# Performance work log

Measured on AMD Instinct MI355X. Metric: run time of the kernel, lower is better.

The kernel has to match this reference:

```python
import jax, jax.numpy as jnp
import numpy as np

L, D, H, T, DFF = 4, 1024, 8, 1000, 4096
HS = D // H  # 128


def _rope_cos_sin():
    # theta_i = 10000^(-2(i-1)/dim) for i in 1..dim/2 (dim = head size)
    i = jnp.arange(1, HS // 2 + 1, dtype=jnp.float32)
    theta = jnp.power(jnp.float32(10000.0), -2.0 * (i - 1.0) / HS)
    t = jnp.arange(T, dtype=jnp.float32)
    ang = t[:, None] * theta[None, :]              # (T, HS/2)
    return jnp.cos(ang), jnp.sin(ang)


def _apply_rope(x, cos, sin):
    # x: (B,H,T,HS); interpret last dim as HS/2 complex pairs and multiply by e^{i t theta}
    xs = x.reshape(*x.shape[:-1], HS // 2, 2)
    xr, xi = xs[..., 0], xs[..., 1]
    c = cos[None, None, :, :]
    s = sin[None, None, :, :]
    out_r = xr * c - xi * s
    out_i = xr * s + xi * c
    return jnp.stack([out_r, out_i], axis=-1).reshape(x.shape)


def _ln(x, g, b, eps=1e-5):
    m = jnp.mean(x, axis=-1, keepdims=True)
    v = jnp.mean((x - m) ** 2, axis=-1, keepdims=True)
    return (x - m) * jax.lax.rsqrt(v + eps) * g + b


def setup_inputs() -> dict:
    key = jax.random.key(0)
    ks = jax.random.split(key, 16)
    sc = 0.02
    inp = {
        'x':   jax.random.normal(ks[0], (8, T, D), jnp.float32),
        'Wq':  sc * jax.random.normal(ks[1], (L, D, D), jnp.float32),
        'Wk':  sc * jax.random.normal(ks[2], (L, D, D), jnp.float32),
        'Wv':  sc * jax.random.normal(ks[3], (L, D, D), jnp.float32),
        'Wpk': sc * jax.random.normal(ks[4], (L, T, T), jnp.float32),
        'bpk': jnp.zeros((L, T), jnp.float32),
        'Wpv': sc * jax.random.normal(ks[5], (L, T, T), jnp.float32),
        'bpv': jnp.zeros((L, T), jnp.float32),
        'ln1_g': jnp.ones((L, D), jnp.float32),
        'ln1_b': jnp.zeros((L, D), jnp.float32),
        'W1':  sc * jax.random.normal(ks[6], (L, DFF, D), jnp.float32),
        'b1':  jnp.zeros((L, DFF), jnp.float32),
        'W2':  sc * jax.random.normal(ks[7], (L, D, DFF), jnp.float32),
        'b2':  jnp.zeros((L, D), jnp.float32),
        'ln2_g': jnp.ones((L, D), jnp.float32),
        'ln2_b': jnp.zeros((L, D), jnp.float32),
    }
    return inp


def reference(x, Wq, Wk, Wv, Wpk, bpk, Wpv, bpv, ln1_g, ln1_b,
              W1, b1, W2, b2, ln2_g, ln2_b):
    B = x.shape[0]
    cos, sin = _rope_cos_sin()
    out = x
    for l in range(L):
        src = out
        # QKV projections (bias=False), split into heads: (B,H,T,HS)
        q = jnp.einsum('btc,dc->btd', src, Wq[l]).reshape(B, T, H, HS).transpose(0, 2, 1, 3)
        k = jnp.einsum('btc,dc->btd', src, Wk[l]).reshape(B, T, H, HS).transpose(0, 2, 1, 3)
        v = jnp.einsum('btc,dc->btd', src, Wv[l]).reshape(B, T, H, HS).transpose(0, 2, 1, 3)
        # ChunkedLinear over the SEQUENCE axis for K and V (single 1000x1000 block)
        k = jnp.einsum('bhtd,ut->bhud', k, Wpk[l]) + bpk[l][None, None, :, None]
        v = jnp.einsum('bhtd,ut->bhud', v, Wpv[l]) + bpv[l][None, None, :, None]
        # RoPE on q and k
        q = _apply_rope(q, cos, sin)
        k = _apply_rope(k, cos, sin)
        # Full (non-causal; mask is commented out in source) softmax attention
        scores = jnp.einsum('bhqd,bhkd->bhqk', q, k) / jnp.sqrt(jnp.float32(HS))
        attn = jax.nn.softmax(scores, axis=-1)
        y = jnp.einsum('bhqk,bhkd->bhqd', attn, v)
        y = y.transpose(0, 2, 1, 3).reshape(B, T, D)  # NOTE: no output proj (faithful to source)
        src = _ln(src + y, ln1_g[l], ln1_b[l])
        h = jax.nn.gelu(jnp.einsum('btd,fd->btf', src, W1[l]) + b1[l], approximate=False)
        src = _ln(src + jnp.einsum('btf,df->btd', h, W2[l]) + b2[l], ln2_g[l], ln2_b[l])
        out = src
    return out
```

## Files before the change

### kernel.cpp

```cpp
#include <hip/hip_runtime.h>
#include <cstdint>
#include <cstddef>


typedef unsigned short u16;
typedef unsigned int u32;
typedef __attribute__((ext_vector_type(8))) short s16x8;
typedef __attribute__((ext_vector_type(4))) float f32x4;
typedef __attribute__((ext_vector_type(4))) unsigned short u16x4;

#define DEV static __device__ __forceinline__

DEV float bf2f(u16 u) { union { u32 u; float f; } v; v.u = ((u32)u) << 16; return v.f; }
DEV u16 f2bf(float f) {
  union { float f; u32 u; } v; v.f = f;
  return (u16)((v.u + 0x7fffu + ((v.u >> 16) & 1u)) >> 16);
}

#define MFMA(acc_, a_, b_) \
  asm volatile("v_mfma_f32_16x16x32_bf16 %0, %1, %2, %0" : "+v"(acc_) : "v"(a_), "v"(b_))

#define GLD16(g_, l_) \
  __builtin_amdgcn_global_load_lds((const __attribute__((address_space(1))) void*)(g_), \
                                   (__attribute__((address_space(3))) void*)(l_), 16, 0, 0)

static constexpr int T_ = 1000, D_ = 1024, H_ = 8, HS_ = 128, B_ = 8;
static constexpr int BT_ = B_ * T_;

DEV void rope8(s16x8& v, const float* __restrict__ ct, const float* __restrict__ st,
               int t, int i0) {
  const f32x4 c4 = *(const f32x4*)(ct + t * 64 + i0);
  const f32x4 s4 = *(const f32x4*)(st + t * 64 + i0);
#pragma unroll
  for (int p = 0; p < 4; ++p) {
    const float xr = bf2f((u16)v[2 * p]), xi = bf2f((u16)v[2 * p + 1]);
    v[2 * p]     = (short)f2bf(xr * c4[p] - xi * s4[p]);
    v[2 * p + 1] = (short)f2bf(xr * s4[p] + xi * c4[p]);
  }
}

__global__ void tab_kernel(float* __restrict__ ct, float* __restrict__ st) {
  const int id = blockIdx.x * 256 + threadIdx.x;
  const int i = id & 63, t = id >> 6;
  const float theta = powf(10000.f, -(float)i * (1.f / 64.f));
  const float ang = (float)t * theta;
  ct[id] = cosf(ang);
  st[id] = sinf(ang);
}

__global__ void convert_kernel(const float* __restrict__ in, u16* __restrict__ out, int n) {
  const int i = (blockIdx.x * 256 + threadIdx.x) * 4;
  if (i < n) {
    const float4 v = *(const float4*)(in + i);
    uint2 pk;
    pk.x = (u32)f2bf(v.x) | ((u32)f2bf(v.y) << 16);
    pk.y = (u32)f2bf(v.z) | ((u32)f2bf(v.w) << 16);
    *(uint2*)(out + i) = pk;
  }
}

__global__ void zerotail_kernel(u16* __restrict__ KTg, u16* __restrict__ VTg,
                                u16* __restrict__ Vmt) {
  const int id = blockIdx.x * 256 + threadIdx.x;
  if (id >= 3 * 8192 * 24) return;
  const int which = id / 196608, rem = id % 196608;
  const int bd = rem / 24, t = 1000 + rem % 24;
  u16* p = (which == 0) ? KTg : (which == 1) ? VTg : Vmt;
  p[(size_t)bd * 1024 + t] = 0;
}

template <int BIAS, bool ACT, bool OUTBF, bool SPLIT>
__global__ __launch_bounds__(256) void gemm2p(
    const u16* __restrict__ A, const u16* __restrict__ B, void* __restrict__ Cv,
    const float* __restrict__ bias, u16* __restrict__ KT, u16* __restrict__ VT,
    int M, int N, int K, int lda, int ldb, int ldc, long sA, long sB, long sC) {
  __shared__ alignas(16) u16 As[2][4096];
  __shared__ alignas(16) u16 Bs[2][4096];
  const int z = blockIdx.z;
  A += (size_t)z * (size_t)sA;
  B += (size_t)z * (size_t)sB;
  const int m0 = blockIdx.y * 128, n0 = blockIdx.x * 128;
  const int tid = threadIdx.x;
  const int wid = tid >> 6, lane = tid & 63;
  const int wr = wid >> 1, wc = wid & 1;
  const int l15 = lane & 15, l4 = lane >> 4;
  const int srow = tid >> 2;
  const int sg = ((tid & 3) ^ ((tid >> 3) & 3)) << 3;
  const u16* gA0 = A + (size_t)min(m0 + srow, M - 1) * lda + sg;
  const u16* gA1 = A + (size_t)min(m0 + 64 + srow, M - 1) * lda + sg;
  const u16* gB0 = B + (size_t)min(n0 + srow, N - 1) * ldb + sg;
  const u16* gB1 = B + (size_t)min(n0 + 64 + srow, N - 1) * ldb + sg;
  const int gg = (l4 ^ ((l15 >> 1) & 3)) << 3;
  const int aBase = (wr * 64 + l15) * 32 + gg;
  const int bBase = (wc * 64 + l15) * 32 + gg;

  f32x4 acc[4][4] = {};
  const int KT_n = K >> 5;
  GLD16(gA0, &As[0][tid * 8]);
  GLD16(gA1, &As[0][(256 + tid) * 8]);
  GLD16(gB0, &Bs[0][tid * 8]);
  GLD16(gB1, &Bs[0][(256 + tid) * 8]);
  __syncthreads();
  int cur = 0;
#pragma unroll 1
  for (int kt = 0; kt < KT_n; ++kt) {
    if (kt + 1 < KT_n) {
      const int kb = (kt + 1) << 5;
      GLD16(gA0 + kb, &As[cur ^ 1][tid * 8]);
      GLD16(gA1 + kb, &As[cur ^ 1][(256 + tid) * 8]);
      GLD16(gB0 + kb, &Bs[cur ^ 1][tid * 8]);
      GLD16(gB1 + kb, &Bs[cur ^ 1][(256 + tid) * 8]);
    }
    s16x8 af[4], bfr[4];
#pragma unroll
    for (int i = 0; i < 4; ++i) af[i] = *(const s16x8*)&As[cur][aBase + i * 512];
#pragma unroll
    for (int i = 0; i < 4; ++i) bfr[i] = *(const s16x8*)&Bs[cur][bBase + i * 512];
    __builtin_amdgcn_s_setprio(1);
#pragma unroll
    for (int mi = 0; mi < 4; ++mi)
#pragma unroll
      for (int ni = 0; ni < 4; ++ni) MFMA(acc[mi][ni], af[mi], bfr[ni]);
    __builtin_amdgcn_s_setprio(0);
    __syncthreads();
    cur ^= 1;
  }
  asm volatile("s_nop 7\n\ts_nop 7"
               : "+v"(acc[3][0]), "+v"(acc[3][1]), "+v"(acc[3][2]), "+v"(acc[3][3]));
  if constexpr (SPLIT) {
#pragma unroll
    for (int mi = 0; mi < 4; ++mi) {
      const int rb = m0 + wr * 64 + mi * 16 + l4 * 4;
      if (rb < M) {
#pragma unroll
        for (int ni = 0; ni < 4; ++ni) {
          const int colg = n0 + wc * 64 + ni * 16 + l15;
          if (colg < 1024) {
#pragma unroll
            for (int r = 0; r < 4; ++r)
              ((u16*)Cv)[(size_t)(rb + r) * 1024 + colg] = f2bf(acc[mi][ni][r]);
          } else {
            u16* dst = (colg < 2048) ? KT : VT;
            const int dcol = colg & 1023;
            const int bq = rb / 1000;
            const int tq = rb - bq * 1000;
            u16x4 pk;
#pragma unroll
            for (int r = 0; r < 4; ++r) pk[r] = f2bf(acc[mi][ni][r]);
            *(u16x4*)(dst + (size_t)bq * 1048576 + (size_t)dcol * 1024 + tq) = pk;
          }
        }
      }
    }
  } else {
#pragma unroll
    for (int mi = 0; mi < 4; ++mi) {
#pragma unroll
      for (int ni = 0; ni < 4; ++ni) {
        const int colg = n0 + wc * 64 + ni * 16 + l15;
#pragma unroll
        for (int r = 0; r < 4; ++r) {
          const int rowg = m0 + wr * 64 + mi * 16 + l4 * 4 + r;
          if (rowg < M && colg < N) {
            float v = acc[mi][ni][r];
            if (BIAS == 1) v += bias[rowg];
            if (BIAS == 2) v += bias[colg];
            if (ACT) v = 0.5f * v * (1.0f + erff(v * 0.70710678118654752f));
            const size_t idx = (size_t)z * (size_t)sC + (size_t)rowg * ldc + colg;
            if (OUTBF) ((u16*)Cv)[idx] = f2bf(v);
            else       ((float*)Cv)[idx] = v;
          }
        }
      }
    }
  }
}

__global__ __launch_bounds__(256) void attn_kernel(const u16* __restrict__ Q,
                                                   const u16* __restrict__ Km,
                                                   const u16* __restrict__ Vmt,
                                                   u16* __restrict__ Y,
                                                   const float* __restrict__ ct,
                                                   const float* __restrict__ st) {
  __shared__ alignas(16) u16 Ks[64][136];
  __shared__ alignas(16) u16 Vts[128][72];
  __shared__ alignas(16) u16 Ps[4][32][72];
  const int qt = blockIdx.x;
  const int bh = blockIdx.y;
  const int b = bh >> 3, h = bh & 7;
  const int tid = threadIdx.x;
  const int w = tid >> 6, lane = tid & 63;
  const int l15 = lane & 15, l4 = lane >> 4;
  const size_t qbase = (size_t)b * 1000 * 1024 + h * HS_;
  const size_t kbase = (size_t)b * 1024000 + h * HS_;
  const size_t vbase = (size_t)b * 1048576 + (size_t)(h * HS_) * 1024;
  const int q0 = qt * 128 + w * 32;
  s16x8 aq[2][4];
#pragma unroll
  for (int qf = 0; qf < 2; ++qf) {
    const int qrow = q0 + qf * 16 + l15;
#pragma unroll
    for (int c = 0; c < 4; ++c) {
      s16x8 v = {};
      if (qrow < T_) {
        v = *(const s16x8*)(Q + qbase + (size_t)qrow * 1024 + c * 32 + l4 * 8);
        rope8(v, ct, st, qrow, c * 16 + l4 * 4);
      }
      aq[qf][c] = v;
    }
  }
  f32x4 acc[2][8] = {};
  float m_run[2][4], l_run[2][4];
#pragma unroll
  for (int qf = 0; qf < 2; ++qf)
#pragma unroll
    for (int r = 0; r < 4; ++r) { m_run[qf][r] = -1e30f; l_run[qf][r] = 0.f; }
  const float SCALE = 0.08838834764831845f;
  for (int kt = 0; kt < 16; ++kt) {
    {
      const int r = tid >> 2, c0 = (tid & 3) << 5;
      const int kk = kt * 64 + r;
#pragma unroll
      for (int v = 0; v < 4; ++v) {
        s16x8 val = {};
        if (kk < T_) {
          val = *(const s16x8*)(Km + kbase + (size_t)kk * 1024 + c0 + v * 8);
          rope8(val, ct, st, kk, (c0 + v * 8) >> 1);
        }
        *(s16x8*)&Ks[r][c0 + v * 8] = val;
      }
      const int r2 = tid >> 1, c2s = (tid & 1) << 5;
#pragma unroll
      for (int v = 0; v < 4; ++v) {
        const s16x8 val = *(const s16x8*)(Vmt + vbase + (size_t)r2 * 1024 + kt * 64 + c2s + v * 8);
        *(s16x8*)&Vts[r2][c2s + v * 8] = val;
      }
    }
    __syncthreads();
    f32x4 sacc[2][4] = {};
#pragma unroll
    for (int c = 0; c < 4; ++c) {
      s16x8 bk[4];
#pragma unroll
      for (int f = 0; f < 4; ++f) bk[f] = *(const s16x8*)&Ks[f * 16 + l15][c * 32 + l4 * 8];
#pragma unroll
      for (int qf = 0; qf < 2; ++qf)
#pragma unroll
        for (int f = 0; f < 4; ++f) MFMA(sacc[qf][f], aq[qf][c], bk[f]);
    }
    asm volatile("s_nop 7\n\ts_nop 7"
                 : "+v"(sacc[0][0]), "+v"(sacc[0][1]), "+v"(sacc[0][2]), "+v"(sacc[0][3]),
                   "+v"(sacc[1][0]), "+v"(sacc[1][1]), "+v"(sacc[1][2]), "+v"(sacc[1][3]));
#pragma unroll
    for (int qf = 0; qf < 2; ++qf) {
      float sv[4][4];
#pragma unroll
      for (int f = 0; f < 4; ++f) {
        const int key = kt * 64 + f * 16 + l15;
#pragma unroll
        for (int r = 0; r < 4; ++r) sv[f][r] = (key < T_) ? sacc[qf][f][r] * SCALE : -1e30f;
      }
#pragma unroll
      for (int r = 0; r < 4; ++r) {
        float mx = fmaxf(fmaxf(sv[0][r], sv[1][r]), fmaxf(sv[2][r], sv[3][r]));
#pragma unroll
        for (int off = 8; off >= 1; off >>= 1) mx = fmaxf(mx, __shfl_xor(mx, off));
        const float mn = fmaxf(m_run[qf][r], mx);
        const float corr = __expf(m_run[qf][r] - mn);
        m_run[qf][r] = mn;
        float rs = 0.f;
#pragma unroll
        for (int f = 0; f < 4; ++f) {
          const float p = __expf(sv[f][r] - mn);
          rs += p;
          Ps[w][qf * 16 + l4 * 4 + r][f * 16 + l15] = f2bf(p);
        }
#pragma unroll
        for (int off = 8; off >= 1; off >>= 1) rs += __shfl_xor(rs, off);
        l_run[qf][r] = l_run[qf][r] * corr + rs;
#pragma unroll
        for (int n = 0; n < 8; ++n) acc[qf][n][r] *= corr;
      }
    }
    asm volatile("s_waitcnt lgkmcnt(0)" ::: "memory");
#pragma unroll
    for (int c2 = 0; c2 < 2; ++c2) {
      s16x8 pa[2];
#pragma unroll
      for (int qf = 0; qf < 2; ++qf)
        pa[qf] = *(const s16x8*)&Ps[w][qf * 16 + l15][c2 * 32 + l4 * 8];
#pragma unroll
      for (int n = 0; n < 8; ++n) {
        const s16x8 vb = *(const s16x8*)&Vts[n * 16 + l15][c2 * 32 + l4 * 8];
#pragma unroll
        for (int qf = 0; qf < 2; ++qf) MFMA(acc[qf][n], pa[qf], vb);
      }
    }
    __syncthreads();
  }
  asm volatile("s_nop 7\n\ts_nop 7"
               : "+v"(acc[0][6]), "+v"(acc[0][7]), "+v"(acc[1][6]), "+v"(acc[1][7]));
#pragma unroll
  for (int qf = 0; qf < 2; ++qf)
#pragma unroll
    for (int n = 0; n < 8; ++n)
#pragma unroll
      for (int r = 0; r < 4; ++r) {
        const int q = q0 + qf * 16 + l4 * 4 + r;
        if (q < T_)
          Y[(size_t)(b * 1000 + q) * 1024 + h * HS_ + n * 16 + l15] =
              f2bf(acc[qf][n][r] / l_run[qf][r]);
      }
}

__global__ __launch_bounds__(256) void addln_kernel(float* __restrict__ src,
                                                    const u16* __restrict__ add,
                                                    const float* __restrict__ g,
                                                    const float* __restrict__ bb,
                                                    u16* __restrict__ outb) {
  const int row = blockIdx.x;
  const int tid = threadIdx.x;
  const int d = tid * 4;
  float* s = src + (size_t)row * D_;
  const u16* a = add + (size_t)row * D_;
  f32x4 sv = *(const f32x4*)(s + d);
  const u16x4 av = *(const u16x4*)(a + d);
  float x[4];
  float sum = 0.f, sq = 0.f;
#pragma unroll
  for (int i = 0; i < 4; ++i) {
    const float v = sv[i] + bf2f(av[i]);
    x[i] = v; sum += v; sq += v * v;
  }
#pragma unroll
  for (int off = 32; off >= 1; off >>= 1) { sum += __shfl_xor(sum, off); sq += __shfl_xor(sq, off); }
  __shared__ float red[8];
  const int wid = tid >> 6;
  if ((tid & 63) == 0) { red[wid] = sum; red[4 + wid] = sq; }
  __syncthreads();
  sum = red[0] + red[1] + red[2] + red[3];
  sq = red[4] + red[5] + red[6] + red[7];
  const float mean = sum * (1.f / 1024.f);
  const float var = sq * (1.f / 1024.f) - mean * mean;
  const float rstd = rsqrtf(var + 1e-5f);
  const f32x4 gv = *(const f32x4*)(g + d);
  const f32x4 bv = *(const f32x4*)(bb + d);
  f32x4 yv;
  u16x4 ob;
#pragma unroll
  for (int i = 0; i < 4; ++i) {
    const float y = (x[i] - mean) * rstd * gv[i] + bv[i];
    yv[i] = y;
    ob[i] = f2bf(y);
  }
  *(f32x4*)(s + d) = yv;
  *(u16x4*)(outb + (size_t)row * D_ + d) = ob;
}

static inline int cdiv(int a, int b) { return (a + b - 1) / b; }

extern "C" void kernel_launch(void* const* d_in, const int* in_sizes, int n_in,
                              void* d_out, int out_size, void* d_ws, size_t ws_size,
                              hipStream_t stream) {
  const float* x    = (const float*)d_in[0];
  const float* Wq   = (const float*)d_in[1];
  const float* Wk   = (const float*)d_in[2];
  const float* Wv   = (const float*)d_in[3];
  const float* Wpk  = (const float*)d_in[4];
  const float* bpk  = (const float*)d_in[5];
  const float* Wpv  = (const float*)d_in[6];
  const float* bpv  = (const float*)d_in[7];
  const float* g1   = (const float*)d_in[8];
  const float* b1ln = (const float*)d_in[9];
  const float* W1   = (const float*)d_in[10];
  const float* b1   = (const float*)d_in[11];
  const float* W2   = (const float*)d_in[12];
  const float* b2   = (const float*)d_in[13];
  const float* g2   = (const float*)d_in[14];
  const float* b2ln = (const float*)d_in[15];

  char* wsb = (char*)d_ws;
  float* cosT = (float*)(wsb + 0);
  float* sinT = (float*)(wsb + 262144);
  float* srcf = (float*)(wsb + 524288);
  u16* srcb   = (u16*)(wsb + 33292288);
  u16* Qb     = (u16*)(wsb + 49676288);
  u16* KTg    = (u16*)(wsb + 66060288);
  u16* VTg    = (u16*)(wsb + 82837504);
  u16* Km     = (u16*)(wsb + 99614720);
  u16* Vmt    = (u16*)(wsb + 115998720);
  u16* yB     = (u16*)(wsb + 132775936);
  u16* wbuf   = (u16*)(wsb + 149159936);
  u16* hB     = Qb;

  u16* wqB  = wbuf + 0;
  u16* wpkB = wbuf + 3145728;
  u16* wpvB = wbuf + 4145728;
  u16* w1B  = wbuf + 5145728;
  u16* w2B  = wbuf + 9340032;

  tab_kernel<<<250, 256, 0, stream>>>(cosT, sinT);
  zerotail_kernel<<<2304, 256, 0, stream>>>(KTg, VTg, Vmt);
  hipMemcpyAsync(srcf, x, (size_t)BT_ * D_ * sizeof(float), hipMemcpyDeviceToDevice, stream);
  convert_kernel<<<cdiv(BT_ * D_, 1024), 256, 0, stream>>>(x, srcb, BT_ * D_);

  for (int l = 0; l < 4; ++l) {
    convert_kernel<<<cdiv(1048576, 1024), 256, 0, stream>>>(Wq + (size_t)l * 1048576, wqB, 1048576);
    convert_kernel<<<cdiv(1048576, 1024), 256, 0, stream>>>(Wk + (size_t)l * 1048576, wqB + 1048576, 1048576);
    convert_kernel<<<cdiv(1048576, 1024), 256, 0, stream>>>(Wv + (size_t)l * 1048576, wqB + 2097152, 1048576);
    convert_kernel<<<cdiv(1000000, 1024), 256, 0, stream>>>(Wpk + (size_t)l * 1000000, wpkB, 1000000);
    convert_kernel<<<cdiv(1000000, 1024), 256, 0, stream>>>(Wpv + (size_t)l * 1000000, wpvB, 1000000);
    convert_kernel<<<cdiv(4194304, 1024), 256, 0, stream>>>(W1 + (size_t)l * 4194304, w1B, 4194304);
    convert_kernel<<<cdiv(4194304, 1024), 256, 0, stream>>>(W2 + (size_t)l * 4194304, w2B, 4194304);

    gemm2p<0, false, true, true><<<dim3(24, 63, 1), 256, 0, stream>>>(
        srcb, wqB, Qb, nullptr, KTg, VTg, BT_, 3072, 1024, 1024, 1024, 1024, 0, 0, 0);

    gemm2p<1, false, true, false><<<dim3(8, 8, 8), 256, 0, stream>>>(
        wpkB, KTg, Km, bpk + (size_t)l * 1000, nullptr, nullptr,
        1000, 1024, 1024, 1000, 1024, 1024, 0L, 1048576L, 1024000L);

    gemm2p<2, false, true, false><<<dim3(8, 8, 8), 256, 0, stream>>>(
        VTg, wpvB, Vmt, bpv + (size_t)l * 1000, nullptr, nullptr,
        1024, 1000, 1024, 1024, 1000, 1024, 1048576L, 0L, 1048576L);

    attn_kernel<<<dim3(8, 64), 256, 0, stream>>>(Qb, Km, Vmt, yB, cosT, sinT);

    addln_kernel<<<BT_, 256, 0, stream>>>(srcf, yB, g1 + (size_t)l * 1024,
                                          b1ln + (size_t)l * 1024, srcb);

    gemm2p<2, true, true, false><<<dim3(32, 63, 1), 256, 0, stream>>>(
        srcb, w1B, hB, b1 + (size_t)l * 4096, nullptr, nullptr,
        BT_, 4096, 1024, 1024, 1024, 4096, 0, 0, 0);
    gemm2p<2, false, true, false><<<dim3(8, 63, 1), 256, 0, stream>>>(
        hB, w2B, yB, b2 + (size_t)l * 1024, nullptr, nullptr,
        BT_, 1024, 4096, 4096, 4096, 1024, 0, 0, 0);

    addln_kernel<<<BT_, 256, 0, stream>>>(srcf, yB, g2 + (size_t)l * 1024,
                                          b2ln + (size_t)l * 1024, srcb);
  }

  hipMemcpyAsync(d_out, srcf, (size_t)BT_ * D_ * sizeof(float), hipMemcpyDeviceToDevice, stream);
}
```

Measured before the change: 2.205 ms.

## Add 256x256 GEMM kernel with XCD-aware block remap and fuse K RoPE into projection

```diff
diff --git a/kernel.cpp b/kernel.cpp
--- a/kernel.cpp
+++ b/kernel.cpp
@@ -69,11 +69,124 @@
   p[(size_t)bd * 1024 + t] = 0;
 }
 
-template <int BIAS, bool ACT, bool OUTBF, bool SPLIT>
+template <int BMT, int BIAS, bool ACT, bool SPLIT>
+__global__ __launch_bounds__(512) void gemm256(
+    const u16* __restrict__ A, const u16* __restrict__ B, u16* __restrict__ Cv,
+    const float* __restrict__ bias, u16* __restrict__ KT, u16* __restrict__ VT,
+    int M, int N, int K, int lda, int ldb, int ldc, int cx, int cy, int ncx) {
+  constexpr int MI = 4 * BMT;
+  __shared__ alignas(16) u16 As[2][BMT * 4096];
+  __shared__ alignas(16) u16 Bs[2][8192];
+  int bx = blockIdx.x, by = blockIdx.y;
+  if (cx) {
+    const int lin = by * gridDim.x + bx;
+    const int xcd = lin & 7, c2 = lin >> 3;
+    bx = (xcd % ncx) * cx + c2 % cx;
+    by = (xcd / ncx) * cy + c2 / cx;
+  }
+  const int m0 = by * (BMT * 128), n0 = bx * 256;
+  const int tid = threadIdx.x;
+  const int wid = tid >> 6, lane = tid & 63;
+  const int wr = wid >> 2, wc = wid & 3;
+  const int l15 = lane & 15, l4 = lane >> 4;
+  const int srow = tid >> 2;
+  const int sg = ((tid & 3) ^ ((tid >> 3) & 3)) << 3;
+  const u16* gA[BMT];
+#pragma unroll
+  for (int j = 0; j < BMT; ++j)
+    gA[j] = A + (size_t)min(m0 + j * 128 + srow, M - 1) * lda + sg;
+  const u16* gB0 = B + (size_t)min(n0 + srow, N - 1) * ldb + sg;
+  const u16* gB1 = B + (size_t)min(n0 + 128 + srow, N - 1) * ldb + sg;
+  const int gg = (l4 ^ ((l15 >> 1) & 3)) << 3;
+  const int aBase = (wr * (BMT * 64) + l15) * 32 + gg;
+  const int bBase = (wc * 64 + l15) * 32 + gg;
+
+  f32x4 acc[MI][4] = {};
+  const int KTn = K >> 5;
+#pragma unroll
+  for (int j = 0; j < BMT; ++j) GLD16(gA[j], &As[0][j * 4096 + tid * 8]);
+  GLD16(gB0, &Bs[0][tid * 8]);
+  GLD16(gB1, &Bs[0][4096 + tid * 8]);
+  __syncthreads();
+  int cur = 0;
+#pragma unroll 1
+  for (int kt = 0; kt < KTn; ++kt) {
+    if (kt + 1 < KTn) {
+      const int kb = (kt + 1) << 5;
+#pragma unroll
+      for (int j = 0; j < BMT; ++j) GLD16(gA[j] + kb, &As[cur ^ 1][j * 4096 + tid * 8]);
+      GLD16(gB0 + kb, &Bs[cur ^ 1][tid * 8]);
+      GLD16(gB1 + kb, &Bs[cur ^ 1][4096 + tid * 8]);
+    }
+    s16x8 af[MI], bfr[4];
+#pragma unroll
+    for (int i = 0; i < MI; ++i) af[i] = *(const s16x8*)&As[cur][aBase + i * 512];
+#pragma unroll
+    for (int i = 0; i < 4; ++i) bfr[i] = *(const s16x8*)&Bs[cur][bBase + i * 512];
+    __builtin_amdgcn_s_setprio(1);
+#pragma unroll
+    for (int mi = 0; mi < MI; ++mi)
+#pragma unroll
+      for (int ni = 0; ni < 4; ++ni) MFMA(acc[mi][ni], af[mi], bfr[ni]);
+    __builtin_amdgcn_s_setprio(0);
+    __syncthreads();
+    cur ^= 1;
+  }
+  asm volatile("s_nop 7\n\ts_nop 7"
+               : "+v"(acc[MI - 1][0]), "+v"(acc[MI - 1][1]),
+                 "+v"(acc[MI - 1][2]), "+v"(acc[MI - 1][3]));
+  if constexpr (SPLIT) {
+#pragma unroll
+    for (int mi = 0; mi < MI; ++mi) {
+      const int rb = m0 + wr * (BMT * 64) + mi * 16 + l4 * 4;
+      if (rb < M) {
+#pragma unroll
+        for (int ni = 0; ni < 4; ++ni) {
+          const int colg = n0 + wc * 64 + ni * 16 + l15;
+          if (colg < 1024) {
+#pragma unroll
+            for (int r = 0; r < 4; ++r)
+              Cv[(size_t)(rb + r) * 1024 + colg] = f2bf(acc[mi][ni][r]);
+          } else {
+            u16* dst = (colg < 2048) ? KT : VT;
+            const int dcol = colg & 1023;
+            const int bq = rb / 1000;
+            const int tq = rb - bq * 1000;
+            u16x4 pk;
+#pragma unroll
+            for (int r = 0; r < 4; ++r) pk[r] = f2bf(acc[mi][ni][r]);
+            *(u16x4*)(dst + (size_t)bq * 1048576 + (size_t)dcol * 1024 + tq) = pk;
+          }
+        }
+      }
+    }
+  } else {
+#pragma unroll
+    for (int mi = 0; mi < MI; ++mi) {
+#pragma unroll
+      for (int ni = 0; ni < 4; ++ni) {
+        const int colg = n0 + wc * 64 + ni * 16 + l15;
+#pragma unroll
+        for (int r = 0; r < 4; ++r) {
+          const int rowg = m0 + wr * (BMT * 64) + mi * 16 + l4 * 4 + r;
+          if (rowg < M) {
+            float v = acc[mi][ni][r];
+            if (BIAS == 2) v += bias[colg];
+            if (ACT) v = 0.5f * v * (1.0f + erff(v * 0.70710678118654752f));
+            Cv[(size_t)rowg * ldc + colg] = f2bf(v);
+          }
+        }
+      }
+    }
+  }
+}
+
+template <int BIAS, bool ACT, bool OUTBF, bool RK>
 __global__ __launch_bounds__(256) void gemm2p(
     const u16* __restrict__ A, const u16* __restrict__ B, void* __restrict__ Cv,
-    const float* __restrict__ bias, u16* __restrict__ KT, u16* __restrict__ VT,
-    int M, int N, int K, int lda, int ldb, int ldc, long sA, long sB, long sC) {
+    const float* __restrict__ bias, const float* __restrict__ ct,
+    const float* __restrict__ st, int M, int N, int K, int lda, int ldb, int ldc,
+    long sA, long sB, long sC) {
   __shared__ alignas(16) u16 As[2][4096];
   __shared__ alignas(16) u16 Bs[2][4096];
   const int z = blockIdx.z;
@@ -95,7 +208,7 @@
   const int bBase = (wc * 64 + l15) * 32 + gg;
 
   f32x4 acc[4][4] = {};
-  const int KT_n = K >> 5;
+  const int KTn = K >> 5;
   GLD16(gA0, &As[0][tid * 8]);
   GLD16(gA1, &As[0][(256 + tid) * 8]);
   GLD16(gB0, &Bs[0][tid * 8]);
@@ -103,8 +216,8 @@
   __syncthreads();
   int cur = 0;
 #pragma unroll 1
-  for (int kt = 0; kt < KT_n; ++kt) {
-    if (kt + 1 < KT_n) {
+  for (int kt = 0; kt < KTn; ++kt) {
+    if (kt + 1 < KTn) {
       const int kb = (kt + 1) << 5;
       GLD16(gA0 + kb, &As[cur ^ 1][tid * 8]);
       GLD16(gA1 + kb, &As[cur ^ 1][(256 + tid) * 8]);
@@ -127,49 +240,29 @@
   }
   asm volatile("s_nop 7\n\ts_nop 7"
                : "+v"(acc[3][0]), "+v"(acc[3][1]), "+v"(acc[3][2]), "+v"(acc[3][3]));
-  if constexpr (SPLIT) {
-#pragma unroll
-    for (int mi = 0; mi < 4; ++mi) {
-      const int rb = m0 + wr * 64 + mi * 16 + l4 * 4;
-      if (rb < M) {
-#pragma unroll
-        for (int ni = 0; ni < 4; ++ni) {
-          const int colg = n0 + wc * 64 + ni * 16 + l15;
-          if (colg < 1024) {
-#pragma unroll
-            for (int r = 0; r < 4; ++r)
-              ((u16*)Cv)[(size_t)(rb + r) * 1024 + colg] = f2bf(acc[mi][ni][r]);
-          } else {
-            u16* dst = (colg < 2048) ? KT : VT;
-            const int dcol = colg & 1023;
-            const int bq = rb / 1000;
-            const int tq = rb - bq * 1000;
-            u16x4 pk;
-#pragma unroll
-            for (int r = 0; r < 4; ++r) pk[r] = f2bf(acc[mi][ni][r]);
-            *(u16x4*)(dst + (size_t)bq * 1048576 + (size_t)dcol * 1024 + tq) = pk;
-          }
+#pragma unroll
+  for (int mi = 0; mi < 4; ++mi) {
+#pragma unroll
+    for (int ni = 0; ni < 4; ++ni) {
+      const int colg = n0 + wc * 64 + ni * 16 + l15;
+#pragma unroll
+      for (int r = 0; r < 4; ++r) {
+        const int rowg = m0 + wr * 64 + mi * 16 + l4 * 4 + r;
+        float v = acc[mi][ni][r];
+        if (BIAS == 1) v += bias[min(rowg, M - 1)];
+        if (BIAS == 2) v += bias[colg];
+        if constexpr (RK) {
+          const int tt = min(rowg, T_ - 1);
+          const int ii = (colg & 127) >> 1;
+          const float c = ct[tt * 64 + ii], s = st[tt * 64 + ii];
+          const float partner = __shfl_xor(v, 1);
+          v = (colg & 1) ? (partner * s + v * c) : (v * c - partner * s);
         }
-      }
-    }
-  } else {
-#pragma unroll
-    for (int mi = 0; mi < 4; ++mi) {
-#pragma unroll
-      for (int ni = 0; ni < 4; ++ni) {
-        const int colg = n0 + wc * 64 + ni * 16 + l15;
-#pragma unroll
-        for (int r = 0; r < 4; ++r) {
-          const int rowg = m0 + wr * 64 + mi * 16 + l4 * 4 + r;
-          if (rowg < M && colg < N) {
-            float v = acc[mi][ni][r];
-            if (BIAS == 1) v += bias[rowg];
-            if (BIAS == 2) v += bias[colg];
-            if (ACT) v = 0.5f * v * (1.0f + erff(v * 0.70710678118654752f));
-            const size_t idx = (size_t)z * (size_t)sC + (size_t)rowg * ldc + colg;
-            if (OUTBF) ((u16*)Cv)[idx] = f2bf(v);
-            else       ((float*)Cv)[idx] = v;
-          }
+        if (ACT) v = 0.5f * v * (1.0f + erff(v * 0.70710678118654752f));
+        if (rowg < M && colg < N) {
+          const size_t idx = (size_t)z * (size_t)sC + (size_t)rowg * ldc + colg;
+          if (OUTBF) ((u16*)Cv)[idx] = f2bf(v);
+          else       ((float*)Cv)[idx] = v;
         }
       }
     }
@@ -223,10 +316,7 @@
 #pragma unroll
       for (int v = 0; v < 4; ++v) {
         s16x8 val = {};
-        if (kk < T_) {
-          val = *(const s16x8*)(Km + kbase + (size_t)kk * 1024 + c0 + v * 8);
-          rope8(val, ct, st, kk, (c0 + v * 8) >> 1);
-        }
+        if (kk < T_) val = *(const s16x8*)(Km + kbase + (size_t)kk * 1024 + c0 + v * 8);
         *(s16x8*)&Ks[r][c0 + v * 8] = val;
       }
       const int r2 = tid >> 1, c2s = (tid & 1) << 5;
@@ -413,11 +503,11 @@
     convert_kernel<<<cdiv(4194304, 1024), 256, 0, stream>>>(W1 + (size_t)l * 4194304, w1B, 4194304);
     convert_kernel<<<cdiv(4194304, 1024), 256, 0, stream>>>(W2 + (size_t)l * 4194304, w2B, 4194304);
 
-    gemm2p<0, false, true, true><<<dim3(24, 63, 1), 256, 0, stream>>>(
-        srcb, wqB, Qb, nullptr, KTg, VTg, BT_, 3072, 1024, 1024, 1024, 1024, 0, 0, 0);
-
-    gemm2p<1, false, true, false><<<dim3(8, 8, 8), 256, 0, stream>>>(
-        wpkB, KTg, Km, bpk + (size_t)l * 1000, nullptr, nullptr,
+    gemm256<2, 0, false, true><<<dim3(12, 32), 512, 0, stream>>>(
+        srcb, wqB, Qb, nullptr, KTg, VTg, BT_, 3072, 1024, 1024, 1024, 1024, 6, 8, 2);
+
+    gemm2p<1, false, true, true><<<dim3(8, 8, 8), 256, 0, stream>>>(
+        wpkB, KTg, Km, bpk + (size_t)l * 1000, cosT, sinT,
         1000, 1024, 1024, 1000, 1024, 1024, 0L, 1048576L, 1024000L);
 
     gemm2p<2, false, true, false><<<dim3(8, 8, 8), 256, 0, stream>>>(
@@ -429,10 +519,10 @@
     addln_kernel<<<BT_, 256, 0, stream>>>(srcf, yB, g1 + (size_t)l * 1024,
                                           b1ln + (size_t)l * 1024, srcb);
 
-    gemm2p<2, true, true, false><<<dim3(32, 63, 1), 256, 0, stream>>>(
+    gemm256<2, 2, true, false><<<dim3(16, 32), 512, 0, stream>>>(
         srcb, w1B, hB, b1 + (size_t)l * 4096, nullptr, nullptr,
-        BT_, 4096, 1024, 1024, 1024, 4096, 0, 0, 0);
-    gemm2p<2, false, true, false><<<dim3(8, 63, 1), 256, 0, stream>>>(
+        BT_, 4096, 1024, 1024, 1024, 4096, 8, 8, 2);
+    gemm256<1, 2, false, false><<<dim3(4, 63), 512, 0, stream>>>(
         hB, w2B, yB, b2 + (size_t)l * 1024, nullptr, nullptr,
         BT_, 1024, 4096, 4096, 4096, 1024, 0, 0, 0);
 
```

After: 2.611 ms. 18.4% more time.

## Fuse weight conversions, apply K RoPE in GEMM epilogue, MFMA row sums

Applied to the files above, without the earlier changes.

```diff
diff --git a/kernel.cpp b/kernel.cpp
--- a/kernel.cpp
+++ b/kernel.cpp
@@ -59,6 +59,29 @@
   }
 }
 
+__global__ __launch_bounds__(256) void convertL_kernel(
+    const float* __restrict__ Wq, const float* __restrict__ Wk, const float* __restrict__ Wv,
+    const float* __restrict__ Wpk, const float* __restrict__ Wpv,
+    const float* __restrict__ W1, const float* __restrict__ W2,
+    u16* __restrict__ wq, u16* __restrict__ wpk, u16* __restrict__ wpv,
+    u16* __restrict__ w1, u16* __restrict__ w2) {
+  const int i = blockIdx.x * 256 + threadIdx.x;
+  const float* src; u16* dst; int j;
+  if      (i <  262144) { src = Wq;  dst = wq;            j = i; }
+  else if (i <  524288) { src = Wk;  dst = wq + 1048576;  j = i -  262144; }
+  else if (i <  786432) { src = Wv;  dst = wq + 2097152;  j = i -  524288; }
+  else if (i < 1036432) { src = Wpk; dst = wpk;           j = i -  786432; }
+  else if (i < 1286432) { src = Wpv; dst = wpv;           j = i - 1036432; }
+  else if (i < 2335008) { src = W1;  dst = w1;            j = i - 1286432; }
+  else if (i < 3383584) { src = W2;  dst = w2;            j = i - 2335008; }
+  else return;
+  const float4 v = ((const float4*)src)[j];
+  uint2 pk;
+  pk.x = (u32)f2bf(v.x) | ((u32)f2bf(v.y) << 16);
+  pk.y = (u32)f2bf(v.z) | ((u32)f2bf(v.w) << 16);
+  ((uint2*)dst)[j] = pk;
+}
+
 __global__ void zerotail_kernel(u16* __restrict__ KTg, u16* __restrict__ VTg,
                                 u16* __restrict__ Vmt) {
   const int id = blockIdx.x * 256 + threadIdx.x;
@@ -69,10 +92,11 @@
   p[(size_t)bd * 1024 + t] = 0;
 }
 
-template <int BIAS, bool ACT, bool OUTBF, bool SPLIT>
+template <int BIAS, bool ACT, bool RK, bool SPLIT>
 __global__ __launch_bounds__(256) void gemm2p(
-    const u16* __restrict__ A, const u16* __restrict__ B, void* __restrict__ Cv,
-    const float* __restrict__ bias, u16* __restrict__ KT, u16* __restrict__ VT,
+    const u16* __restrict__ A, const u16* __restrict__ B, u16* __restrict__ Cv,
+    const float* __restrict__ bias, const float* __restrict__ ct,
+    const float* __restrict__ st, u16* __restrict__ KT, u16* __restrict__ VT,
     int M, int N, int K, int lda, int ldb, int ldc, long sA, long sB, long sC) {
   __shared__ alignas(16) u16 As[2][4096];
   __shared__ alignas(16) u16 Bs[2][4096];
@@ -95,7 +119,7 @@
   const int bBase = (wc * 64 + l15) * 32 + gg;
 
   f32x4 acc[4][4] = {};
-  const int KT_n = K >> 5;
+  const int KTn = K >> 5;
   GLD16(gA0, &As[0][tid * 8]);
   GLD16(gA1, &As[0][(256 + tid) * 8]);
   GLD16(gB0, &Bs[0][tid * 8]);
@@ -103,8 +127,8 @@
   __syncthreads();
   int cur = 0;
 #pragma unroll 1
-  for (int kt = 0; kt < KT_n; ++kt) {
-    if (kt + 1 < KT_n) {
+  for (int kt = 0; kt < KTn; ++kt) {
+    if (kt + 1 < KTn) {
       const int kb = (kt + 1) << 5;
       GLD16(gA0 + kb, &As[cur ^ 1][tid * 8]);
       GLD16(gA1 + kb, &As[cur ^ 1][(256 + tid) * 8]);
@@ -138,7 +162,7 @@
           if (colg < 1024) {
 #pragma unroll
             for (int r = 0; r < 4; ++r)
-              ((u16*)Cv)[(size_t)(rb + r) * 1024 + colg] = f2bf(acc[mi][ni][r]);
+              Cv[(size_t)(rb + r) * 1024 + colg] = f2bf(acc[mi][ni][r]);
           } else {
             u16* dst = (colg < 2048) ? KT : VT;
             const int dcol = colg & 1023;
@@ -161,15 +185,19 @@
 #pragma unroll
         for (int r = 0; r < 4; ++r) {
           const int rowg = m0 + wr * 64 + mi * 16 + l4 * 4 + r;
-          if (rowg < M && colg < N) {
-            float v = acc[mi][ni][r];
-            if (BIAS == 1) v += bias[rowg];
-            if (BIAS == 2) v += bias[colg];
-            if (ACT) v = 0.5f * v * (1.0f + erff(v * 0.70710678118654752f));
-            const size_t idx = (size_t)z * (size_t)sC + (size_t)rowg * ldc + colg;
-            if (OUTBF) ((u16*)Cv)[idx] = f2bf(v);
-            else       ((float*)Cv)[idx] = v;
+          float v = acc[mi][ni][r];
+          if (BIAS == 1) v += bias[min(rowg, M - 1)];
+          if (BIAS == 2) v += bias[min(colg, N - 1)];
+          if constexpr (RK) {
+            const int tt = min(rowg, T_ - 1);
+            const int ii = (colg & 127) >> 1;
+            const float c = ct[tt * 64 + ii], s = st[tt * 64 + ii];
+            const float partner = __shfl_xor(v, 1);
+            v = (colg & 1) ? (partner * s + v * c) : (v * c - partner * s);
           }
+          if (ACT) v = 0.5f * v * (1.0f + erff(v * 0.70710678118654752f));
+          if (rowg < M && colg < N)
+            Cv[(size_t)z * (size_t)sC + (size_t)rowg * ldc + colg] = f2bf(v);
         }
       }
     }
@@ -209,12 +237,16 @@
       aq[qf][c] = v;
     }
   }
+  s16x8 ones;
+#pragma unroll
+  for (int j = 0; j < 8; ++j) ones[j] = (short)0x3F80;
   f32x4 acc[2][8] = {};
-  float m_run[2][4], l_run[2][4];
+  f32x4 lsum[2] = {};
+  float m_run[2][4];
 #pragma unroll
   for (int qf = 0; qf < 2; ++qf)
 #pragma unroll
-    for (int r = 0; r < 4; ++r) { m_run[qf][r] = -1e30f; l_run[qf][r] = 0.f; }
+    for (int r = 0; r < 4; ++r) m_run[qf][r] = -1e30f;
   const float SCALE = 0.08838834764831845f;
   for (int kt = 0; kt < 16; ++kt) {
     {
@@ -223,10 +255,7 @@
 #pragma unroll
       for (int v = 0; v < 4; ++v) {
         s16x8 val = {};
-        if (kk < T_) {
-          val = *(const s16x8*)(Km + kbase + (size_t)kk * 1024 + c0 + v * 8);
-          rope8(val, ct, st, kk, (c0 + v * 8) >> 1);
-        }
+        if (kk < T_) val = *(const s16x8*)(Km + kbase + (size_t)kk * 1024 + c0 + v * 8);
         *(s16x8*)&Ks[r][c0 + v * 8] = val;
       }
       const int r2 = tid >> 1, c2s = (tid & 1) << 5;
@@ -268,16 +297,10 @@
         const float mn = fmaxf(m_run[qf][r], mx);
         const float corr = __expf(m_run[qf][r] - mn);
         m_run[qf][r] = mn;
-        float rs = 0.f;
-#pragma unroll
-        for (int f = 0; f < 4; ++f) {
-          const float p = __expf(sv[f][r] - mn);
-          rs += p;
-          Ps[w][qf * 16 + l4 * 4 + r][f * 16 + l15] = f2bf(p);
-        }
-#pragma unroll
-        for (int off = 8; off >= 1; off >>= 1) rs += __shfl_xor(rs, off);
-        l_run[qf][r] = l_run[qf][r] * corr + rs;
+#pragma unroll
+        for (int f = 0; f < 4; ++f)
+          Ps[w][qf * 16 + l4 * 4 + r][f * 16 + l15] = f2bf(__expf(sv[f][r] - mn));
+        lsum[qf][r] *= corr;
 #pragma unroll
         for (int n = 0; n < 8; ++n) acc[qf][n][r] *= corr;
       }
@@ -289,6 +312,8 @@
 #pragma unroll
       for (int qf = 0; qf < 2; ++qf)
         pa[qf] = *(const s16x8*)&Ps[w][qf * 16 + l15][c2 * 32 + l4 * 8];
+      MFMA(lsum[0], pa[0], ones);
+      MFMA(lsum[1], pa[1], ones);
 #pragma unroll
       for (int n = 0; n < 8; ++n) {
         const s16x8 vb = *(const s16x8*)&Vts[n * 16 + l15][c2 * 32 + l4 * 8];
@@ -299,7 +324,8 @@
     __syncthreads();
   }
   asm volatile("s_nop 7\n\ts_nop 7"
-               : "+v"(acc[0][6]), "+v"(acc[0][7]), "+v"(acc[1][6]), "+v"(acc[1][7]));
+               : "+v"(acc[0][6]), "+v"(acc[0][7]), "+v"(acc[1][6]), "+v"(acc[1][7]),
+                 "+v"(lsum[0]), "+v"(lsum[1]));
 #pragma unroll
   for (int qf = 0; qf < 2; ++qf)
 #pragma unroll
@@ -309,7 +335,7 @@
         const int q = q0 + qf * 16 + l4 * 4 + r;
         if (q < T_)
           Y[(size_t)(b * 1000 + q) * 1024 + h * HS_ + n * 16 + l15] =
-              f2bf(acc[qf][n][r] / l_run[qf][r]);
+              f2bf(acc[qf][n][r] / lsum[qf][r]);
       }
 }
 
@@ -405,23 +431,22 @@
   convert_kernel<<<cdiv(BT_ * D_, 1024), 256, 0, stream>>>(x, srcb, BT_ * D_);
 
   for (int l = 0; l < 4; ++l) {
-    convert_kernel<<<cdiv(1048576, 1024), 256, 0, stream>>>(Wq + (size_t)l * 1048576, wqB, 1048576);
-    convert_kernel<<<cdiv(1048576, 1024), 256, 0, stream>>>(Wk + (size_t)l * 1048576, wqB + 1048576, 1048576);
-    convert_kernel<<<cdiv(1048576, 1024), 256, 0, stream>>>(Wv + (size_t)l * 1048576, wqB + 2097152, 1048576);
-    convert_kernel<<<cdiv(1000000, 1024), 256, 0, stream>>>(Wpk + (size_t)l * 1000000, wpkB, 1000000);
-    convert_kernel<<<cdiv(1000000, 1024), 256, 0, stream>>>(Wpv + (size_t)l * 1000000, wpvB, 1000000);
-    convert_kernel<<<cdiv(4194304, 1024), 256, 0, stream>>>(W1 + (size_t)l * 4194304, w1B, 4194304);
-    convert_kernel<<<cdiv(4194304, 1024), 256, 0, stream>>>(W2 + (size_t)l * 4194304, w2B, 4194304);
-
-    gemm2p<0, false, true, true><<<dim3(24, 63, 1), 256, 0, stream>>>(
-        srcb, wqB, Qb, nullptr, KTg, VTg, BT_, 3072, 1024, 1024, 1024, 1024, 0, 0, 0);
+    convertL_kernel<<<13218, 256, 0, stream>>>(
+        Wq + (size_t)l * 1048576, Wk + (size_t)l * 1048576, Wv + (size_t)l * 1048576,
+        Wpk + (size_t)l * 1000000, Wpv + (size_t)l * 1000000,
+        W1 + (size_t)l * 4194304, W2 + (size_t)l * 4194304,
+        wqB, wpkB, wpvB, w1B, w2B);
+
+    gemm2p<0, false, false, true><<<dim3(24, 63, 1), 256, 0, stream>>>(
+        srcb, wqB, Qb, nullptr, nullptr, nullptr, KTg, VTg,
+        BT_, 3072, 1024, 1024, 1024, 1024, 0, 0, 0);
 
     gemm2p<1, false, true, false><<<dim3(8, 8, 8), 256, 0, stream>>>(
-        wpkB, KTg, Km, bpk + (size_t)l * 1000, nullptr, nullptr,
+        wpkB, KTg, Km, bpk + (size_t)l * 1000, cosT, sinT, nullptr, nullptr,
         1000, 1024, 1024, 1000, 1024, 1024, 0L, 1048576L, 1024000L);
 
-    gemm2p<2, false, true, false><<<dim3(8, 8, 8), 256, 0, stream>>>(
-        VTg, wpvB, Vmt, bpv + (size_t)l * 1000, nullptr, nullptr,
+    gemm2p<2, false, false, false><<<dim3(8, 8, 8), 256, 0, stream>>>(
+        VTg, wpvB, Vmt, bpv + (size_t)l * 1000, nullptr, nullptr, nullptr, nullptr,
         1024, 1000, 1024, 1024, 1000, 1024, 1048576L, 0L, 1048576L);
 
     attn_kernel<<<dim3(8, 64), 256, 0, stream>>>(Qb, Km, Vmt, yB, cosT, sinT);
@@ -429,11 +454,11 @@
     addln_kernel<<<BT_, 256, 0, stream>>>(srcf, yB, g1 + (size_t)l * 1024,
                                           b1ln + (size_t)l * 1024, srcb);
 
-    gemm2p<2, true, true, false><<<dim3(32, 63, 1), 256, 0, stream>>>(
-        srcb, w1B, hB, b1 + (size_t)l * 4096, nullptr, nullptr,
+    gemm2p<2, true, false, false><<<dim3(32, 63, 1), 256, 0, stream>>>(
+        srcb, w1B, hB, b1 + (size_t)l * 4096, nullptr, nullptr, nullptr, nullptr,
         BT_, 4096, 1024, 1024, 1024, 4096, 0, 0, 0);
-    gemm2p<2, false, true, false><<<dim3(8, 63, 1), 256, 0, stream>>>(
-        hB, w2B, yB, b2 + (size_t)l * 1024, nullptr, nullptr,
+    gemm2p<2, false, false, false><<<dim3(8, 63, 1), 256, 0, stream>>>(
+        hB, w2B, yB, b2 + (size_t)l * 1024, nullptr, nullptr, nullptr, nullptr,
         BT_, 1024, 4096, 4096, 4096, 1024, 0, 0, 0);
 
     addln_kernel<<<BT_, 256, 0, stream>>>(srcf, yB, g2 + (size_t)l * 1024,
```

Measured after the change: 2.111 ms. 4.3% less time.
